# Kernel tuning notes

Hardware: AMD Instinct MI355X
Metric: run time of the kernel (lower is better)

Reference implementation:

```python
import jax, jax.numpy as jnp
import numpy as np

N = 4096
DEG = 16.0
KC = 64  # max closed-neighborhood size supported (deg~16 graph => safe)


def setup_inputs() -> dict:
    key = jax.random.key(0)
    ks = jax.random.split(key, 6)
    u = jax.random.uniform(ks[0], (N, N))
    upper = jnp.triu((u < (DEG / N)).astype(jnp.float32), k=1)
    adj = upper + upper.T  # symmetric 0/1, zero diagonal
    d = 64
    return {
        'adj': adj,
        'e_w': jax.random.normal(ks[1], (15, d), dtype=jnp.float32) * 0.25,
        'e_b': jnp.zeros((d,), jnp.float32),
        'w1': jax.random.normal(ks[2], (3, d, d), dtype=jnp.float32) * 0.125,
        'b1': jnp.zeros((3, d), jnp.float32),
        'w2': jax.random.normal(ks[3], (3, d, d), dtype=jnp.float32) * 0.125,
        'b2': jnp.zeros((3, d), jnp.float32),
        'eps': jnp.zeros((3,), jnp.float32),
    }


def cr_feat(adj):
    n = adj.shape[0]
    m = adj + jnp.eye(n, dtype=adj.dtype)  # closed-neighborhood indicator rows [N,N]
    k = m.sum(1)                            # |S_v|
    D = m @ adj                             # D[v,u] = degree of u inside S_v (A symmetric)
    E = 0.5 * jnp.sum(m * D, axis=1)        # edges inside S_v
    W = jnp.sum(m * D * (D - 1.0) * 0.5, axis=1)  # wedges inside S_v
    vals, idx = jax.lax.top_k(m, KC)        # members of S_v (padded)
    valid = (vals > 0.5).astype(adj.dtype)
    sub = adj[idx[:, :, None], idx[:, None, :]]        # [N,KC,KC] induced subgraph
    sub = sub * valid[:, :, None] * valid[:, None, :]
    T = jnp.einsum('vij,vjk,vki->v', sub, sub, sub) / 6.0  # triangles inside S_v
    f3 = T
    f2 = W - 3.0 * T
    f1 = E * (k - 2.0) - 2.0 * f2 - 3.0 * f3
    tot = k * (k - 1.0) * (k - 2.0) / 6.0   # C(k,3) = total triples
    f0 = tot - f1 - f2 - f3
    f = jnp.stack([f0, f1, f2, f3], axis=1)
    f = jnp.where((k >= 3.0)[:, None], f, 0.0)  # original skips |nb|<3
    return f / (jnp.sum(f, axis=1, keepdims=True) + 1e-10)


def ww_feat(adj):
    a2 = adj @ adj
    a4 = a2 @ a2                             # matrix_power(adj, 4)
    vals, _ = jax.lax.top_k(a4, 8)           # per-row sort desc, top 8
    return vals


def degree_feat(adj):
    d = adj.sum(1)
    diag_a2 = jnp.einsum('vu,uv->v', adj, adj)  # diag(A@A)
    return jnp.stack([d, d ** 2, diag_a2], axis=1)


def _forward(adj, e_w, e_b, w1, b1, w2, b2, eps):
    feats = jnp.concatenate([cr_feat(adj), ww_feat(adj), degree_feat(adj)], axis=1)  # [N,15]
    x = feats @ e_w + e_b
    for i in range(3):
        h = (1.0 + eps[i]) * x + adj @ x
        x = jax.nn.relu(h @ w1[i] + b1[i]) @ w2[i] + b2[i]
    return x.sum(0)


def reference(adj, e_w, e_b, w1, b1, w2, b2, eps):
    return _forward(adj, e_w, e_b, w1, b1, w2, b2, eps)
```

## Files before the change

kernel.cpp:

```cpp
#include <hip/hip_runtime.h>
#include <hip/hip_bf16.h>
#include <stdint.h>

#define NN 4096


__global__ __launch_bounds__(256) void scan_k(const float* __restrict__ adj,
                                              int* __restrict__ nbr,
                                              int* __restrict__ deg,
                                              unsigned long long* __restrict__ abits,
                                              float* __restrict__ feats) {
    __shared__ int nlist[4][64];
    int tid = threadIdx.x;
    int wv = tid >> 6, ln = tid & 63;
    int v = blockIdx.x * 4 + wv;
    size_t rb = (size_t)v * NN;
    int total = 0;
    unsigned long long w0 = 0;
    const float4* row4 = (const float4*)(adj + rb);
    for (int base = 0; base < NN; base += 256) {
        float4 f = row4[(base >> 2) + ln];
        int q4 = (base >> 8) << 2;
        #pragma unroll
        for (int j = 0; j < 4; j++) {
            float vj = (j == 0) ? f.x : (j == 1) ? f.y : (j == 2) ? f.z : f.w;
            unsigned long long m = __ballot(vj > 0.5f);
            if (vj > 0.5f) {
                int pos = total + __popcll(m & ((1ull << ln) - 1ull));
                if (pos < 64) nlist[wv][pos] = base + 4 * ln + j;
            }
            if (ln == q4 + j) w0 = m;
            total += __popcll(m);
        }
    }
    abits[(size_t)v * 64 + ln] = w0;
    int degL = min(total, 64);
    if (ln < degL) nbr[v * 64 + ln] = nlist[wv][ln];
    if (ln == 0) {
        deg[v] = total;
        float degf = (float)total;
        feats[v * 16 + 12] = degf;
        feats[v * 16 + 13] = degf * degf;
        feats[v * 16 + 14] = degf;
    }
}

__global__ __launch_bounds__(256) void cra2_k(const unsigned long long* __restrict__ abits,
                                              const int* __restrict__ nbr,
                                              const int* __restrict__ deg,
                                              unsigned int* __restrict__ a3n,
                                              unsigned int* __restrict__ side,
                                              unsigned int* __restrict__ scnt,
                                              float* __restrict__ feats) {
    __shared__ __align__(64) unsigned int smem[NN + 132 + 640];
    int tid = threadIdx.x;
    int bid = blockIdx.x;
    int wv = tid >> 6, ln = tid & 63;

    if (bid < NN) {
        unsigned int* acc   = smem;
        int* us             = (int*)(smem + NN);
        int* dus            = (int*)(smem + NN + 64);
        unsigned int* wsumS = smem + NN + 128;
        unsigned int* srcL  = smem + NN + 132;
        int v = bid;
        uint4 z = {0u, 0u, 0u, 0u};
        #pragma unroll
        for (int i = 0; i < 4; i++) ((uint4*)acc)[tid + 256 * i] = z;
        int dv = min(deg[v], 64);
        if (tid < dv) {
            int u = nbr[v * 64 + tid];
            us[tid] = u;
            dus[tid] = min(deg[u], 64);
        }
        __syncthreads();
        for (int p = tid; p < dv * 64; p += 256) {
            int i = p >> 6, wi = p & 63;
            if (wi < dus[i]) atomicAdd(&acc[nbr[us[i] * 64 + wi]], 1u);
        }
        __syncthreads();
        unsigned int myw[16];
        int local = 0;
        #pragma unroll
        for (int m = 0; m < 16; m++) {
            unsigned int a = acc[tid + 256 * m];
            myw[m] = a;
            local += (a != 0u);
        }
        int incl = local;
        #pragma unroll
        for (int off = 1; off < 64; off <<= 1) {
            int n = __shfl_up(incl, off, 64);
            if (ln >= off) incl += n;
        }
        if (ln == 63) wsumS[wv] = (unsigned int)incl;
        __syncthreads();
        unsigned int wpre = 0, nsrc = 0;
        #pragma unroll
        for (int q = 0; q < 4; q++) {
            unsigned int s = wsumS[q];
            if (q < wv) wpre += s;
            nsrc += s;
        }
        unsigned int pos = wpre + (unsigned int)(incl - local);
        #pragma unroll
        for (int m = 0; m < 16; m++) {
            unsigned int a = myw[m];
            if (a) {
                unsigned int col = (unsigned int)tid + 256u * m;
                unsigned int dgu = (unsigned int)min(deg[col], 64);
                if (pos < 640u) srcL[pos] = (a << 19) | (dgu << 12) | col;
                pos++;
            }
        }
        if (nsrc > 640u) nsrc = 640u;
        __syncthreads();
        #pragma unroll
        for (int i = 0; i < 4; i++) ((uint4*)acc)[tid + 256 * i] = z;
        __syncthreads();
        int lim64 = (((int)nsrc + 1) >> 1) << 6;
        for (int q = tid; q < lim64; q += 256) {
            int s = ((q >> 6) << 1) | ((q >> 5) & 1);
            int j = q & 31;
            if (s < (int)nsrc) {
                unsigned int e = srcL[s];
                int dgu = (int)((e >> 12) & 0x7Fu);
                unsigned int w = e >> 19;
                const int* nru = nbr + (e & 0xFFFu) * 64;
                if (j < dgu) atomicAdd(&acc[nru[j]], w);
                if (j == 31) {
                    for (int jj = 32; jj < dgu; jj++) atomicAdd(&acc[nru[jj]], w);
                }
            }
        }
        __syncthreads();
        unsigned int wAn = 0, wBn = 0, ovm = 0;
        #pragma unroll
        for (int i2 = 0; i2 < 8; i2++) {
            unsigned int a = acc[8 * tid + i2];
            wAn |= min(a, 15u) << (4 * i2);
            ovm |= (a > 15u ? 1u : 0u) << i2;
        }
        #pragma unroll
        for (int i2 = 0; i2 < 8; i2++) {
            unsigned int a = acc[2048 + 8 * tid + i2];
            wBn |= min(a, 15u) << (4 * i2);
            ovm |= (a > 15u ? 1u : 0u) << (8 + i2);
        }
        {
            uint2 nw; nw.x = wAn; nw.y = wBn;
            ((uint2*)((char*)a3n + (size_t)v * 2048))[tid] = nw;
        }
        int lov = __popc(ovm);
        int inc2 = lov;
        #pragma unroll
        for (int off = 1; off < 64; off <<= 1) {
            int n = __shfl_up(inc2, off, 64);
            if (ln >= off) inc2 += n;
        }
        if (ln == 63) wsumS[wv] = (unsigned int)inc2;
        __syncthreads();
        unsigned int wpre2 = 0, totS = 0;
        #pragma unroll
        for (int q = 0; q < 4; q++) {
            unsigned int s = wsumS[q];
            if (q < wv) wpre2 += s;
            totS += s;
        }
        unsigned int pos2 = wpre2 + (unsigned int)(inc2 - lov);
        unsigned int* sideR = side + (size_t)v * 192;
        while (ovm) {
            int i2 = __ffs(ovm) - 1;
            ovm &= ovm - 1;
            unsigned int col = (i2 < 8) ? (unsigned int)(8 * tid + i2)
                                        : (unsigned int)(2048 + 8 * tid + (i2 - 8));
            unsigned int a = acc[col];
            if (pos2 < 192u) sideR[pos2] = ((a - 15u) << 16) | col;
            pos2++;
        }
        if (tid == 0) scnt[v] = min(totS, 192u);
    } else {
        unsigned long long* rows = (unsigned long long*)smem;
        int* mems = (int*)(smem + 1024);
        int v = (bid - NN) * 4 + wv;

        int dv = deg[v];
        int degL = min(dv, 64);
        int c = min(dv + 1, 64);

        int nl = (ln < degL) ? nbr[v * 64 + ln] : 0;
        int isless = (ln < degL && nl < v) ? 1 : 0;
        int pos = isless;
        #pragma unroll
        for (int off = 32; off; off >>= 1) pos += __shfl_xor(pos, off, 64);

        int mem = 0;
        if (ln < c) {
            if (ln < pos)       mem = nl;
            else if (ln == pos) mem = v;
            else                mem = nbr[v * 64 + ln - 1];
        }
        mems[wv * 64 + ln] = mem;
        __syncthreads();

        unsigned long long mask = 0ull;
        {
            const unsigned long long* rowb = abits + (size_t)mem * 64;
            for (int j = 0; j < c; j++) {
                int mj = mems[wv * 64 + j];
                unsigned long long w = rowb[((mj >> 8) << 2) | (mj & 3)];
                mask |= ((w >> ((mj >> 2) & 63)) & 1ull) << j;
            }
        }
        if (ln >= c) mask = 0ull;
        rows[wv * 64 + ln] = mask;
        __syncthreads();

        int tpart = 0;
        float epart = 0.f, wpart = 0.f;
        if (ln < c) {
            unsigned long long mm = mask;
            while (mm) {
                int j = __ffsll(mm) - 1;
                mm &= mm - 1;
                tpart += __popcll(mask & rows[wv * 64 + j]);
            }
            if (ln != pos) {
                int cn = __popcll(rows[wv * 64 + pos] & mask);
                float D2 = (float)cn + 1.0f;
                epart = D2;
                wpart = D2 * (D2 - 1.0f) * 0.5f;
            }
        }
        float es = epart, wsum2 = wpart;
        int ts = tpart;
        #pragma unroll
        for (int off = 32; off; off >>= 1) {
            es += __shfl_xor(es, off, 64);
            wsum2 += __shfl_xor(wsum2, off, 64);
            ts += __shfl_xor(ts, off, 64);
        }

        if (ln == 0) {
            float degf = (float)dv;
            float k = degf + 1.0f;
            float E = 0.5f * (es + degf);
            float W = wsum2 + degf * (degf - 1.0f) * 0.5f;
            float T = (float)ts / 6.0f;
            float f3 = T;
            float f2 = W - 3.0f * T;
            float f1 = E * (k - 2.0f) - 2.0f * f2 - 3.0f * f3;
            float tot2 = k * (k - 1.0f) * (k - 2.0f) / 6.0f;
            float f0 = tot2 - f1 - f2 - f3;
            if (k < 3.0f) { f0 = f1 = f2 = f3 = 0.f; }
            float s = f0 + f1 + f2 + f3 + 1e-10f;
            feats[v * 16 + 0] = f0 / s;
            feats[v * 16 + 1] = f1 / s;
            feats[v * 16 + 2] = f2 / s;
            feats[v * 16 + 3] = f3 / s;
        }
    }
}

__global__ __launch_bounds__(1024) void order_k(const int* __restrict__ deg,
                                                int* __restrict__ ord) {
    __shared__ unsigned int bcnt[192];
    __shared__ unsigned int bbase[192];
    int tid = threadIdx.x;
    if (tid < 192) bcnt[tid] = 0u;
    __syncthreads();
    unsigned char myk[4];
    #pragma unroll
    for (int j = 0; j < 4; j++) {
        int v = tid * 4 + j;
        myk[j] = (unsigned char)min(deg[v], 191);
        atomicAdd(&bcnt[myk[j]], 1u);
    }
    __syncthreads();
    if (tid == 0) {
        unsigned int run = 0;
        for (int b = 191; b >= 0; b--) { bbase[b] = run; run += bcnt[b]; }
    }
    __syncthreads();
    #pragma unroll
    for (int j = 0; j < 4; j++) {
        int v = tid * 4 + j;
        unsigned int p = atomicAdd(&bbase[myk[j]], 1u);
        ord[p] = v;
    }
}

#define DONIB(w, a1e) \
    { unsigned int x_ = (w) & 0x0F0F0F0Fu;                                      \
      unsigned int y_ = ((w) >> 4) & 0x0F0F0F0Fu;                               \
      atomicAdd(&acc[(a1e) ^ 0u], __builtin_amdgcn_perm(y_, x_, 0x0c040c00u));  \
      atomicAdd(&acc[(a1e) ^ 1u], __builtin_amdgcn_perm(y_, x_, 0x0c050c01u));  \
      atomicAdd(&acc[(a1e) ^ 2u], __builtin_amdgcn_perm(y_, x_, 0x0c060c02u));  \
      atomicAdd(&acc[(a1e) ^ 3u], __builtin_amdgcn_perm(y_, x_, 0x0c070c03u)); }

__global__ __launch_bounds__(512) void a4row_k(const uint2* __restrict__ a3n2,
                                               const unsigned int* __restrict__ side,
                                               const unsigned int* __restrict__ scnt,
                                               const int* __restrict__ deg,
                                               const int* __restrict__ nbr,
                                               const int* __restrict__ ord,
                                               const float* __restrict__ feats,
                                               const float* __restrict__ e_w,
                                               const float* __restrict__ e_b,
                                               float* __restrict__ x0) {
    __shared__ __align__(64) unsigned int acc[NN / 2];
    __shared__ unsigned int sbase[64];
    __shared__ unsigned int sS[64];
    __shared__ unsigned int wtops[64];
    int tid = threadIdx.x;
    int wv = tid >> 6, ln = tid & 63;
    int v = ord[blockIdx.x];

    {
        uint4 z = {0u, 0u, 0u, 0u};
        ((uint4*)acc)[tid] = z;
    }
    int dvv = min(deg[v], 64);
    if (tid < dvv) {
        unsigned int u = (unsigned int)nbr[v * 64 + tid];
        sbase[tid] = u;
        sS[tid] = scnt[u];
    }
    __syncthreads();

    int tot1 = dvv << 8;
    for (int g = tid; g < tot1; g += 512) {
        unsigned int q = (unsigned int)g & 255u;
        uint2 W = a3n2[sbase[g >> 8] * 256u + q];
        unsigned int a1e = (q << 2) | ((q >> 3) & 3u);
        DONIB(W.x, a1e)
        DONIB(W.y, a1e + 1024u)
    }
    for (int i = wv; i < dvv; i += 8) {
        int ns = (int)sS[i];
        const unsigned int* sp = side + (size_t)sbase[i] * 192;
        for (int g2 = ln; g2 < ns; g2 += 64) {
            unsigned int e = sp[g2];
            unsigned int col = e & 0xFFFu;
            unsigned int w = e >> 16;
            unsigned int pidx = col >> 1;
            unsigned int ad = pidx ^ ((pidx >> 5) & 3u);
            atomicAdd(&acc[ad], w << ((col & 1u) << 4));
        }
    }
    __syncthreads();

    unsigned int best[8];
    #pragma unroll
    for (int q = 0; q < 8; q++) best[q] = 0u;
    #pragma unroll
    for (int m = 0; m < 4; m++) {
        unsigned int w = acc[tid + 512 * m];
        #pragma unroll
        for (int hlf = 0; hlf < 2; hlf++) {
            unsigned int val = hlf ? (w >> 16) : (w & 0xFFFFu);
            if (val > best[7]) {
                best[7] = val;
                #pragma unroll
                for (int s = 7; s > 0; s--) {
                    if (best[s] > best[s - 1]) {
                        unsigned int t2 = best[s - 1]; best[s - 1] = best[s]; best[s] = t2;
                    } else break;
                }
            }
        }
    }

    unsigned int wave_val = 0u;
    #pragma unroll
    for (int r = 0; r < 8; r++) {
        unsigned int m = best[0];
        #pragma unroll
        for (int off = 32; off; off >>= 1)
            m = max(m, (unsigned int)__shfl_xor((int)m, off, 64));
        unsigned long long bb = __ballot(best[0] == m);
        int src = __ffsll(bb) - 1;
        if (ln == src) {
            #pragma unroll
            for (int s = 0; s < 7; s++) best[s] = best[s + 1];
            best[7] = 0u;
        }
        if (ln == r) wave_val = m;
    }
    if (ln < 8) wtops[wv * 8 + ln] = wave_val;
    __syncthreads();

    if (wv == 0) {
        unsigned int cand = wtops[ln];
        unsigned int myv = 0u;
        #pragma unroll
        for (int r = 0; r < 8; r++) {
            unsigned int m = cand;
            #pragma unroll
            for (int off = 32; off; off >>= 1)
                m = max(m, (unsigned int)__shfl_xor((int)m, off, 64));
            unsigned long long bb = __ballot(cand == m);
            int src = __ffsll(bb) - 1;
            if (ln == src) cand = 0u;
            if (ln == r) myv = m;
        }
        int d = ln;
        float s = e_b[d];
        s += feats[v * 16 + 0]  * e_w[0 * 64 + d];
        s += feats[v * 16 + 1]  * e_w[1 * 64 + d];
        s += feats[v * 16 + 2]  * e_w[2 * 64 + d];
        s += feats[v * 16 + 3]  * e_w[3 * 64 + d];
        #pragma unroll
        for (int j = 0; j < 8; j++) {
            float mj = (float)(unsigned int)__shfl((int)myv, j, 64);
            s += mj * e_w[(4 + j) * 64 + d];
        }
        s += feats[v * 16 + 12] * e_w[12 * 64 + d];
        s += feats[v * 16 + 13] * e_w[13 * 64 + d];
        s += feats[v * 16 + 14] * e_w[14 * 64 + d];
        x0[(size_t)v * 64 + d] = s;
    }
}

__global__ __launch_bounds__(256) void layer_k(const float* __restrict__ xin,
                                               float* __restrict__ xout,
                                               const float* __restrict__ w1,
                                               const float* __restrict__ b1,
                                               const float* __restrict__ w2,
                                               const float* __restrict__ b2,
                                               const float* __restrict__ eps,
                                               const int* __restrict__ nbr,
                                               const int* __restrict__ deg,
                                               float* __restrict__ out,
                                               int li) {
    __shared__ float wL[4096];
    __shared__ float h[4][64], t[4][64];
    int tid = threadIdx.x;
    int wv = tid >> 6, d = tid & 63;
    int v = blockIdx.x * 4 + wv;

    {
        const float4* src = (const float4*)(w1 + li * 4096);
        #pragma unroll
        for (int i = 0; i < 4; i++) ((float4*)wL)[tid + 256 * i] = src[tid + 256 * i];
    }

    float xv = xin[(size_t)v * 64 + d];
    int dv = min(deg[v], 64);
    const int* nl = nbr + v * 64;
    float agg = 0.f;
    int j = 0;
    for (; j + 4 <= dv; j += 4) {
        int n0 = nl[j], n1 = nl[j + 1], n2 = nl[j + 2], n3 = nl[j + 3];
        float a0 = xin[(size_t)n0 * 64 + d];
        float a1 = xin[(size_t)n1 * 64 + d];
        float a2v = xin[(size_t)n2 * 64 + d];
        float a3 = xin[(size_t)n3 * 64 + d];
        agg += (a0 + a1) + (a2v + a3);
    }
    for (; j < dv; j++) agg += xin[(size_t)nl[j] * 64 + d];
    float hv = (1.0f + eps[li]) * xv + agg;
    h[wv][d] = hv;
    __syncthreads();

    float s = b1[li * 64 + d];
    #pragma unroll 8
    for (int k = 0; k < 64; k++) s += h[wv][k] * wL[k * 64 + d];
    s = fmaxf(s, 0.f);
    t[wv][d] = s;
    __syncthreads();

    {
        const float4* src = (const float4*)(w2 + li * 4096);
        #pragma unroll
        for (int i = 0; i < 4; i++) ((float4*)wL)[tid + 256 * i] = src[tid + 256 * i];
    }
    __syncthreads();

    float o = b2[li * 64 + d];
    #pragma unroll 8
    for (int k = 0; k < 64; k++) o += t[wv][k] * wL[k * 64 + d];
    if (li == 2) {
        h[wv][d] = o;
        __syncthreads();
        if (wv == 0)
            atomicAdd(&out[d], (h[0][d] + h[1][d]) + (h[2][d] + h[3][d]));
    } else {
        xout[(size_t)v * 64 + d] = o;
    }
}

extern "C" void kernel_launch(void* const* d_in, const int* in_sizes, int n_in,
                              void* d_out, int out_size, void* d_ws, size_t ws_size,
                              hipStream_t stream) {
    const float* adj = (const float*)d_in[0];
    const float* e_w = (const float*)d_in[1];
    const float* e_b = (const float*)d_in[2];
    const float* w1  = (const float*)d_in[3];
    const float* b1  = (const float*)d_in[4];
    const float* w2  = (const float*)d_in[5];
    const float* b2  = (const float*)d_in[6];
    const float* eps = (const float*)d_in[7];
    float* out = (float*)d_out;

    char* ws = (char*)d_ws;
    unsigned int*       a3n     = (unsigned int*)(ws);
    unsigned int*       side    = (unsigned int*)(ws + 8388608);
    unsigned int*       scnt    = (unsigned int*)(ws + 11534336);
    int*                nbr     = (int*)(ws + 25165824);
    int*                deg     = (int*)(ws + 26214400);
    float*              feats   = (float*)(ws + 26247168);
    float*              x0      = (float*)(ws + 26509312);
    float*              x1      = (float*)(ws + 27557888);
    unsigned long long* abits   = (unsigned long long*)(ws + 28868608);
    int*                ord     = (int*)(ws + 30969856);

    hipMemsetAsync(out, 0, 64 * sizeof(float), stream);
    scan_k<<<1024, 256, 0, stream>>>(adj, nbr, deg, abits, feats);
    cra2_k<<<5120, 256, 0, stream>>>(abits, nbr, deg, a3n, side, scnt, feats);
    order_k<<<1, 1024, 0, stream>>>(deg, ord);
    a4row_k<<<4096, 512, 0, stream>>>((const uint2*)a3n, side, scnt, deg, nbr, ord, feats, e_w, e_b, x0);
    layer_k<<<1024, 256, 0, stream>>>(x0, x1, w1, b1, w2, b2, eps, nbr, deg, out, 0);
    layer_k<<<1024, 256, 0, stream>>>(x1, x0, w1, b1, w2, b2, eps, nbr, deg, out, 1);
    layer_k<<<1024, 256, 0, stream>>>(x0, x1, w1, b1, w2, b2, eps, nbr, deg, out, 2);
}
```

Before: 262.6 us.

## Replace LDS atomic nibble scatter with per-thread register accumulation of A3 rows

Changes the packed 4-bit A^3 row layout so each thread owns 16 contiguous columns. The A^4 row kernel then sums neighbor rows directly in registers with packed SWAR adds, where it used to scatter every nibble into shared memory with atomics. Shared-memory atomics remain only for the overflow side entries, now kept as a full 32-bit-per-column array. This is meant to remove most LDS atomic traffic and its bank conflicts, at the cost of a larger shared buffer and per-chunk unpacking every 16 neighbors to avoid byte overflow.

```diff
diff --git a/kernel.cpp b/kernel.cpp
--- a/kernel.cpp
+++ b/kernel.cpp
@@ -137,19 +137,19 @@
         unsigned int wAn = 0, wBn = 0, ovm = 0;
         #pragma unroll
         for (int i2 = 0; i2 < 8; i2++) {
-            unsigned int a = acc[8 * tid + i2];
+            unsigned int a = acc[16 * tid + i2];
             wAn |= min(a, 15u) << (4 * i2);
             ovm |= (a > 15u ? 1u : 0u) << i2;
         }
         #pragma unroll
         for (int i2 = 0; i2 < 8; i2++) {
-            unsigned int a = acc[2048 + 8 * tid + i2];
+            unsigned int a = acc[16 * tid + 8 + i2];
             wBn |= min(a, 15u) << (4 * i2);
             ovm |= (a > 15u ? 1u : 0u) << (8 + i2);
         }
         {
             uint2 nw; nw.x = wAn; nw.y = wBn;
-            ((uint2*)((char*)a3n + (size_t)v * 2048))[tid] = nw;
+            ((uint2*)(a3n + (size_t)v * 512))[tid] = nw;
         }
         int lov = __popc(ovm);
         int inc2 = lov;
@@ -172,8 +172,7 @@
         while (ovm) {
             int i2 = __ffs(ovm) - 1;
             ovm &= ovm - 1;
-            unsigned int col = (i2 < 8) ? (unsigned int)(8 * tid + i2)
-                                        : (unsigned int)(2048 + 8 * tid + (i2 - 8));
+            unsigned int col = (unsigned int)(16 * tid + i2);
             unsigned int a = acc[col];
             if (pos2 < 192u) sideR[pos2] = ((a - 15u) << 16) | col;
             pos2++;
@@ -290,15 +289,7 @@
     }
 }
 
-#define DONIB(w, a1e) \
-    { unsigned int x_ = (w) & 0x0F0F0F0Fu;                                      \
-      unsigned int y_ = ((w) >> 4) & 0x0F0F0F0Fu;                               \
-      atomicAdd(&acc[(a1e) ^ 0u], __builtin_amdgcn_perm(y_, x_, 0x0c040c00u));  \
-      atomicAdd(&acc[(a1e) ^ 1u], __builtin_amdgcn_perm(y_, x_, 0x0c050c01u));  \
-      atomicAdd(&acc[(a1e) ^ 2u], __builtin_amdgcn_perm(y_, x_, 0x0c060c02u));  \
-      atomicAdd(&acc[(a1e) ^ 3u], __builtin_amdgcn_perm(y_, x_, 0x0c070c03u)); }
-
-__global__ __launch_bounds__(512) void a4row_k(const uint2* __restrict__ a3n2,
+__global__ __launch_bounds__(512) void a4row_k(const unsigned int* __restrict__ a3n,
                                                const unsigned int* __restrict__ side,
                                                const unsigned int* __restrict__ scnt,
                                                const int* __restrict__ deg,
@@ -308,8 +299,9 @@
                                                const float* __restrict__ e_w,
                                                const float* __restrict__ e_b,
                                                float* __restrict__ x0) {
-    __shared__ __align__(64) unsigned int acc[NN / 2];
+    __shared__ unsigned int sacc[NN];
     __shared__ unsigned int sbase[64];
+    __shared__ unsigned int sbs[64];
     __shared__ unsigned int sS[64];
     __shared__ unsigned int wtops[64];
     int tid = threadIdx.x;
@@ -318,55 +310,69 @@
 
     {
         uint4 z = {0u, 0u, 0u, 0u};
-        ((uint4*)acc)[tid] = z;
+        ((uint4*)sacc)[tid] = z;
+        ((uint4*)sacc)[tid + 512] = z;
     }
     int dvv = min(deg[v], 64);
     if (tid < dvv) {
         unsigned int u = (unsigned int)nbr[v * 64 + tid];
-        sbase[tid] = u;
-        sS[tid] = scnt[u];
-    }
-    __syncthreads();
-
-    int tot1 = dvv << 8;
-    for (int g = tid; g < tot1; g += 512) {
-        unsigned int q = (unsigned int)g & 255u;
-        uint2 W = a3n2[sbase[g >> 8] * 256u + q];
-        unsigned int a1e = (q << 2) | ((q >> 3) & 3u);
-        DONIB(W.x, a1e)
-        DONIB(W.y, a1e + 1024u)
-    }
+        sbase[tid] = u * 512u;
+        sbs[tid]   = u * 192u;
+        sS[tid]    = scnt[u];
+    }
+    __syncthreads();
+
     for (int i = wv; i < dvv; i += 8) {
         int ns = (int)sS[i];
-        const unsigned int* sp = side + (size_t)sbase[i] * 192;
+        const unsigned int* sp = side + sbs[i];
         for (int g2 = ln; g2 < ns; g2 += 64) {
             unsigned int e = sp[g2];
-            unsigned int col = e & 0xFFFu;
-            unsigned int w = e >> 16;
-            unsigned int pidx = col >> 1;
-            unsigned int ad = pidx ^ ((pidx >> 5) & 3u);
-            atomicAdd(&acc[ad], w << ((col & 1u) << 4));
-        }
-    }
-    __syncthreads();
+            atomicAdd(&sacc[e & 0xFFFu], e >> 16);
+        }
+    }
+
+    unsigned int aE = 0, aO = 0;
+    unsigned int SE0 = 0, SE1 = 0, SO0 = 0, SO1 = 0;
+    for (int s0 = 0; s0 < dvv; s0 += 16) {
+        int se = min(s0 + 16, dvv);
+        for (int s = s0; s < se; s++) {
+            unsigned int w = a3n[sbase[s] + (unsigned int)tid];
+            aE += w & 0x0F0F0F0Fu;
+            aO += (w >> 4) & 0x0F0F0F0Fu;
+        }
+        SE0 += __builtin_amdgcn_perm(0u, aE, 0x0c010c00u);
+        SE1 += __builtin_amdgcn_perm(0u, aE, 0x0c030c02u);
+        SO0 += __builtin_amdgcn_perm(0u, aO, 0x0c010c00u);
+        SO1 += __builtin_amdgcn_perm(0u, aO, 0x0c030c02u);
+        aE = 0; aO = 0;
+    }
+    __syncthreads();
+
+    uint4 s03 = ((uint4*)sacc)[2 * tid];
+    uint4 s47 = ((uint4*)sacc)[2 * tid + 1];
+    unsigned int vv[8];
+    vv[0] = (SE0 & 0xFFFFu) + s03.x;
+    vv[1] = (SO0 & 0xFFFFu) + s03.y;
+    vv[2] = (SE0 >> 16)     + s03.z;
+    vv[3] = (SO0 >> 16)     + s03.w;
+    vv[4] = (SE1 & 0xFFFFu) + s47.x;
+    vv[5] = (SO1 & 0xFFFFu) + s47.y;
+    vv[6] = (SE1 >> 16)     + s47.z;
+    vv[7] = (SO1 >> 16)     + s47.w;
 
     unsigned int best[8];
     #pragma unroll
     for (int q = 0; q < 8; q++) best[q] = 0u;
     #pragma unroll
-    for (int m = 0; m < 4; m++) {
-        unsigned int w = acc[tid + 512 * m];
-        #pragma unroll
-        for (int hlf = 0; hlf < 2; hlf++) {
-            unsigned int val = hlf ? (w >> 16) : (w & 0xFFFFu);
-            if (val > best[7]) {
-                best[7] = val;
-                #pragma unroll
-                for (int s = 7; s > 0; s--) {
-                    if (best[s] > best[s - 1]) {
-                        unsigned int t2 = best[s - 1]; best[s - 1] = best[s]; best[s] = t2;
-                    } else break;
-                }
+    for (int m = 0; m < 8; m++) {
+        unsigned int val = vv[m];
+        if (val > best[7]) {
+            best[7] = val;
+            #pragma unroll
+            for (int s = 7; s > 0; s--) {
+                if (best[s] > best[s - 1]) {
+                    unsigned int t2 = best[s - 1]; best[s - 1] = best[s]; best[s] = t2;
+                } else break;
             }
         }
     }
@@ -519,7 +525,7 @@
     scan_k<<<1024, 256, 0, stream>>>(adj, nbr, deg, abits, feats);
     cra2_k<<<5120, 256, 0, stream>>>(abits, nbr, deg, a3n, side, scnt, feats);
     order_k<<<1, 1024, 0, stream>>>(deg, ord);
-    a4row_k<<<4096, 512, 0, stream>>>((const uint2*)a3n, side, scnt, deg, nbr, ord, feats, e_w, e_b, x0);
+    a4row_k<<<4096, 512, 0, stream>>>(a3n, side, scnt, deg, nbr, ord, feats, e_w, e_b, x0);
     layer_k<<<1024, 256, 0, stream>>>(x0, x1, w1, b1, w2, b2, eps, nbr, deg, out, 0);
     layer_k<<<1024, 256, 0, stream>>>(x1, x0, w1, b1, w2, b2, eps, nbr, deg, out, 1);
     layer_k<<<1024, 256, 0, stream>>>(x0, x1, w1, b1, w2, b2, eps, nbr, deg, out, 2);
```

Result: no change. 259.7 us (-1.1%).
